# Kernel optimization log

Hardware: AMD Instinct MI355X
Metric: run time of the kernel (lower is better)

## Reference

```python
import jax, jax.numpy as jnp
import numpy as np

B, T, D_MODEL, WINDOW = 2, 2048, 512, 32


def setup_inputs() -> dict:
    key = jax.random.key(0)
    ks = jax.random.split(key, 5)
    s = 1.0 / np.sqrt(D_MODEL)
    x = jax.random.normal(ks[0], (B, T, D_MODEL), jnp.float32)
    # torch.nn.Linear convention: weight [out_features, in_features], y = x @ W.T + b
    w_qkv = jax.random.uniform(ks[1], (3 * D_MODEL, D_MODEL), jnp.float32, -s, s)
    b_qkv = jax.random.uniform(ks[2], (3 * D_MODEL,), jnp.float32, -s, s)
    w_proj = jax.random.uniform(ks[3], (D_MODEL, D_MODEL), jnp.float32, -s, s)
    b_proj = jax.random.uniform(ks[4], (D_MODEL,), jnp.float32, -s, s)
    return {"x": x, "w_qkv": w_qkv, "b_qkv": b_qkv, "w_proj": w_proj, "b_proj": b_proj}


def reference(x, w_qkv, b_qkv, w_proj, b_proj):
    Bb, Tt, C = x.shape
    qkv = x @ w_qkv.T + b_qkv                      # [B,T,3C]
    q, k, v = jnp.split(qkv, 3, axis=-1)           # each [B,T,C]
    W = 2 * WINDOW - 1                             # non-causal window span [t-w+1, t+w-1]
    offs = jnp.arange(W) - (WINDOW - 1)            # [W]
    idx = jnp.arange(Tt)[:, None] + offs[None, :]  # [T,W] absolute key positions
    valid = (idx >= 0) & (idx < Tt)                # mask out-of-range window slots
    idx_c = jnp.clip(idx, 0, Tt - 1)
    k_win = k[:, idx_c]                            # [B,T,W,C]
    v_win = v[:, idx_c]                            # [B,T,W,C]
    scale = jnp.asarray(C, x.dtype) ** 0.5
    scores = jnp.einsum('btc,btwc->btw', q, k_win) / scale
    scores = jnp.where(valid[None], scores, -jnp.inf)
    p = jax.nn.softmax(scores, axis=-1)            # [B,T,W]
    out = jnp.einsum('btw,btwc->btc', p, v_win)    # [B,T,C]
    return out @ w_proj.T + b_proj
```

## Files before the change

### kernel.cpp

```cpp
#include <hip/hip_runtime.h>
#include <math.h>

#define BB 2
#define TT 2048
#define CC 512
#define WIN 32
#define WSZ 63
#define MM (BB * TT)

typedef __attribute__((ext_vector_type(8))) short short8;
typedef __attribute__((ext_vector_type(4))) float floatx4;

__device__ inline unsigned short bf16_rn(float f) {
  unsigned u = __builtin_bit_cast(unsigned, f);
  u += 0x7fff + ((u >> 16) & 1);
  return (unsigned short)(u >> 16);
}
__device__ inline unsigned pack_bf16x2(float lo, float hi) {
  return (unsigned)bf16_rn(lo) | ((unsigned)bf16_rn(hi) << 16);
}

__device__ inline void gll16(const void* g, void* l) {
  __builtin_amdgcn_global_load_lds(
      (const __attribute__((address_space(1))) void*)g,
      (__attribute__((address_space(3))) void*)l, 16, 0, 0);
}

#define NX  (MM * CC)
#define NWQ (3 * CC * CC)
#define NWP (CC * CC)

__global__ __launch_bounds__(256) void convert_bf16(
    const float* __restrict__ x, const float* __restrict__ wq,
    const float* __restrict__ wp, ushort* __restrict__ xb,
    ushort* __restrict__ wqb, ushort* __restrict__ wpb) {
  const size_t e = ((size_t)blockIdx.x * 256 + threadIdx.x) * 8;
  const float* src;
  ushort* dst;
  size_t off;
  if (e < NX) { src = x; dst = xb; off = e; }
  else if (e < NX + NWQ) { src = wq; dst = wqb; off = e - NX; }
  else { src = wp; dst = wpb; off = e - NX - NWQ; }
  float4 v0 = ((const float4*)(src + off))[0];
  float4 v1 = ((const float4*)(src + off))[1];
  uint4 o;
  o.x = pack_bf16x2(v0.x, v0.y);
  o.y = pack_bf16x2(v0.z, v0.w);
  o.z = pack_bf16x2(v1.x, v1.y);
  o.w = pack_bf16x2(v1.z, v1.w);
  *(uint4*)(dst + off) = o;
}

#define GBK 32
#define VTBASE 1024

template <int BN, typename OT>
__global__ __launch_bounds__(256) void gemm_nt_mfma(
    const ushort* __restrict__ A, const ushort* __restrict__ B,
    const float* __restrict__ bias, OT* __restrict__ C,
    ushort* __restrict__ VT, int M, int N, int K) {
  constexpr int NI = 4;
  constexpr int MIW = (BN == 128) ? 4 : 2;
  __shared__ __align__(16) ushort As[128 * GBK];
  __shared__ __align__(16) ushort Bs[BN * GBK];

  const int tid = threadIdx.x;
  const int lane = tid & 63;
  const int wave = tid >> 6;
  const int wm = (BN == 128) ? (wave >> 1) * 64 : wave * 32;
  const int wn = (BN == 128) ? (wave & 1) * 64 : 0;
  const int m0 = blockIdx.y * 128;
  const int n0 = blockIdx.x * BN;
  const int mlane = lane & 15, quad = lane >> 4;
  const int lrow = lane >> 2, lcol = (lane & 3) * 8;

  floatx4 acc[MIW][NI];
#pragma unroll
  for (int i = 0; i < MIW; ++i)
#pragma unroll
    for (int j = 0; j < NI; ++j) acc[i][j] = (floatx4){0.f, 0.f, 0.f, 0.f};

  for (int k0 = 0; k0 < K; k0 += GBK) {
    __syncthreads();
#pragma unroll
    for (int q = 0; q < 2; ++q) {
      const int r0 = (q * 4 + wave) * 16;
      gll16(A + (size_t)(m0 + r0 + lrow) * K + k0 + lcol, As + r0 * GBK);
    }
#pragma unroll
    for (int q = 0; q < BN / 64; ++q) {
      const int r0 = (q * 4 + wave) * 16;
      gll16(B + (size_t)(n0 + r0 + lrow) * K + k0 + lcol, Bs + r0 * GBK);
    }
    __syncthreads();

    short8 af[MIW], bfr[NI];
#pragma unroll
    for (int mi = 0; mi < MIW; ++mi)
      af[mi] = *(const short8*)(&As[(wm + mi * 16 + mlane) * GBK + quad * 8]);
#pragma unroll
    for (int ni = 0; ni < NI; ++ni)
      bfr[ni] = *(const short8*)(&Bs[(wn + ni * 16 + mlane) * GBK + quad * 8]);
#pragma unroll
    for (int mi = 0; mi < MIW; ++mi)
#pragma unroll
      for (int ni = 0; ni < NI; ++ni)
        acc[mi][ni] = __builtin_amdgcn_mfma_f32_16x16x32_bf16(af[mi], bfr[ni], acc[mi][ni], 0, 0, 0);
  }

  const bool vpath = (VT != nullptr) && (n0 >= VTBASE);
#pragma unroll
  for (int ni = 0; ni < NI; ++ni) {
    const int n = n0 + wn + ni * 16 + mlane;
    const float bn = bias[n];
#pragma unroll
    for (int mi = 0; mi < MIW; ++mi) {
      const int mbase = m0 + wm + mi * 16 + quad * 4;
      if (vpath) {
        ushort4 pk;
        pk.x = bf16_rn(acc[mi][ni][0] + bn);
        pk.y = bf16_rn(acc[mi][ni][1] + bn);
        pk.z = bf16_rn(acc[mi][ni][2] + bn);
        pk.w = bf16_rn(acc[mi][ni][3] + bn);
        *(ushort4*)(VT + (size_t)(n - VTBASE) * M + mbase) = pk;
      } else {
#pragma unroll
        for (int r = 0; r < 4; ++r) {
          float val = acc[mi][ni][r] + bn;
          if constexpr (sizeof(OT) == 2)
            ((ushort*)C)[(size_t)(mbase + r) * N + n] = bf16_rn(val);
          else
            ((float*)C)[(size_t)(mbase + r) * N + n] = val;
        }
      }
    }
  }
}

#define ATILE 8
#define SLD 84
#define PLD 104

__global__ __launch_bounds__(256) void attn_mfma(
    const ushort* __restrict__ qkv, const ushort* __restrict__ vT,
    ushort* __restrict__ out) {
  __shared__ __align__(16) float s_s[16 * SLD];
  __shared__ __align__(16) ushort p_s[16 * PLD];

  const int tid = threadIdx.x;
  const int wave = tid >> 6, lane = tid & 63;
  const int mlane = lane & 15, quad = lane >> 4;
  const int bt0 = blockIdx.x * ATILE;
  const int b = bt0 / TT, t0 = bt0 % TT;
  const ushort* qbase = qkv + (size_t)b * TT * (3 * CC);

  const ushort* qrow  = qbase + (ptrdiff_t)(t0 + mlane) * (3 * CC);
  const ushort* krow0 = qbase + (ptrdiff_t)(t0 - 32 + wave * 16 + mlane) * (3 * CC) + CC;
  const ushort* krow1 = qbase + (ptrdiff_t)(t0 - 32 + 64 + mlane) * (3 * CC) + CC;
  floatx4 sacc0 = (floatx4){0.f, 0.f, 0.f, 0.f};
  floatx4 sacc1 = (floatx4){0.f, 0.f, 0.f, 0.f};
#pragma unroll
  for (int ks = 0; ks < 16; ++ks) {
    short8 a  = *(const short8*)(qrow + ks * 32 + quad * 8);
    short8 b0 = *(const short8*)(krow0 + ks * 32 + quad * 8);
    sacc0 = __builtin_amdgcn_mfma_f32_16x16x32_bf16(a, b0, sacc0, 0, 0, 0);
    if (wave == 0) {
      short8 b1 = *(const short8*)(krow1 + ks * 32 + quad * 8);
      sacc1 = __builtin_amdgcn_mfma_f32_16x16x32_bf16(a, b1, sacc1, 0, 0, 0);
    }
  }

#pragma unroll
  for (int r = 0; r < 4; ++r)
    s_s[(quad * 4 + r) * SLD + wave * 16 + mlane] = sacc0[r];
  if (wave == 0) {
#pragma unroll
    for (int r = 0; r < 4; ++r)
      s_s[(quad * 4 + r) * SLD + 64 + mlane] = sacc1[r];
  }
  __syncthreads();

  {
    const int row = tid >> 4, li = tid & 15;
    const float inv_scale = 0.044194173824159216f;
    float e[5];
    float mx = -INFINITY;
#pragma unroll
    for (int i = 0; i < 5; ++i) {
      const int r = li + 16 * i;
      const int j = r - 1 - row;
      const int src = t0 - 32 + r;
      const bool valid = (j >= 0) && (j < WSZ) && (src >= 0) && (src < TT);
      e[i] = valid ? s_s[row * SLD + r] * inv_scale : -INFINITY;
      mx = fmaxf(mx, e[i]);
    }
    mx = fmaxf(mx, __shfl_xor(mx, 1)); mx = fmaxf(mx, __shfl_xor(mx, 2));
    mx = fmaxf(mx, __shfl_xor(mx, 4)); mx = fmaxf(mx, __shfl_xor(mx, 8));
    float sum = 0.f;
#pragma unroll
    for (int i = 0; i < 5; ++i) {
      e[i] = (e[i] == -INFINITY) ? 0.f : __expf(e[i] - mx);
      sum += e[i];
    }
    sum += __shfl_xor(sum, 1); sum += __shfl_xor(sum, 2);
    sum += __shfl_xor(sum, 4); sum += __shfl_xor(sum, 8);
    const float rs = 1.f / sum;
#pragma unroll
    for (int i = 0; i < 5; ++i)
      p_s[row * PLD + li + 16 * i] = bf16_rn(e[i] * rs);
    if (li < 8) {
      p_s[row * PLD + 80 + li] = 0;
      p_s[row * PLD + 88 + li] = 0;
      p_s[row * PLD + 96 + li] = 0;
    }
  }
  __syncthreads();

  const ptrdiff_t mcol0 = (ptrdiff_t)b * TT + t0 - 32;
#pragma unroll 2
  for (int nt8 = 0; nt8 < 8; ++nt8) {
    const int nt = wave * 8 + nt8;
    const ushort* vrow = vT + (ptrdiff_t)(nt * 16 + mlane) * MM + mcol0;
    floatx4 o = (floatx4){0.f, 0.f, 0.f, 0.f};
#pragma unroll
    for (int ks = 0; ks < 3; ++ks) {
      short8 a  = *(const short8*)(&p_s[mlane * PLD + ks * 32 + quad * 8]);
      short8 bv = *(const short8*)(vrow + ks * 32 + quad * 8);
      o = __builtin_amdgcn_mfma_f32_16x16x32_bf16(a, bv, o, 0, 0, 0);
    }
    if (quad < 2) {
#pragma unroll
      for (int r = 0; r < 4; ++r)
        out[(size_t)(bt0 + quad * 4 + r) * CC + nt * 16 + mlane] = bf16_rn(o[r]);
    }
  }
}

extern "C" void kernel_launch(void* const* d_in, const int* in_sizes, int n_in,
                              void* d_out, int out_size, void* d_ws, size_t ws_size,
                              hipStream_t stream) {
  const float* x      = (const float*)d_in[0];
  const float* w_qkv  = (const float*)d_in[1];
  const float* b_qkv  = (const float*)d_in[2];
  const float* w_proj = (const float*)d_in[3];
  const float* b_proj = (const float*)d_in[4];
  float* outp = (float*)d_out;

  ushort* base  = (ushort*)d_ws;
  ushort* qkv   = base + 131072;
  ushort* attn  = qkv + (size_t)MM * 3 * CC;
  ushort* xb    = attn + (size_t)MM * CC;
  ushort* wqb   = xb + (size_t)NX;
  ushort* wpb   = wqb + (size_t)NWQ;
  ushort* vTg   = wpb + (size_t)NWP;
  ushort* vT    = vTg + 64;

  convert_bf16<<<(NX + NWQ + NWP) / (256 * 8), 256, 0, stream>>>(x, w_qkv, w_proj, xb, wqb, wpb);
  {
    dim3 grid((3 * CC) / 128, MM / 128);
    gemm_nt_mfma<128, ushort><<<grid, 256, 0, stream>>>(xb, wqb, b_qkv, qkv, vT, MM, 3 * CC, CC);
  }
  attn_mfma<<<MM / ATILE, 256, 0, stream>>>(qkv, vT, attn);
  {
    dim3 grid(CC / 64, MM / 128);
    gemm_nt_mfma<64, float><<<grid, 256, 0, stream>>>(attn, wpb, b_proj, outp, nullptr, MM, CC, CC);
  }
}
```

Before: 120.5 us.

## Replace GEMM with B-panel-in-LDS kernel reading A directly from global

Rewrites both GEMMs so each block stages a 64-row weight panel (half of K at a time) in padded LDS and streams A fragments straight from global memory into MFMA operands. This removes the per-K-step double barrier and small global-to-LDS loads. Tile shapes change to 128x64 for the QKV GEMM and 64x64 for the projection, which doubles the block count. The V-transpose epilogue now goes through LDS so VT gets coalesced 16-byte stores. The cost is uncached global reads of A with a 64-byte stride per lane, and lower arithmetic intensity per block.

```diff
diff --git a/kernel.cpp b/kernel.cpp
--- a/kernel.cpp
+++ b/kernel.cpp
@@ -18,12 +18,6 @@
 }
 __device__ inline unsigned pack_bf16x2(float lo, float hi) {
   return (unsigned)bf16_rn(lo) | ((unsigned)bf16_rn(hi) << 16);
-}
-
-__device__ inline void gll16(const void* g, void* l) {
-  __builtin_amdgcn_global_load_lds(
-      (const __attribute__((address_space(1))) void*)g,
-      (__attribute__((address_space(3))) void*)l, 16, 0, 0);
 }
 
 #define NX  (MM * CC)
@@ -51,79 +45,67 @@
   *(uint4*)(dst + off) = o;
 }
 
-#define GBK 32
-#define VTBASE 1024
-
-template <int BN, typename OT>
-__global__ __launch_bounds__(256) void gemm_nt_mfma(
+#define PSTR 264
+#define VSTR 136
+
+template <int BM, typename OT>
+__global__ __launch_bounds__(256) void gemm_panel(
     const ushort* __restrict__ A, const ushort* __restrict__ B,
     const float* __restrict__ bias, OT* __restrict__ C,
-    ushort* __restrict__ VT, int M, int N, int K) {
-  constexpr int NI = 4;
-  constexpr int MIW = (BN == 128) ? 4 : 2;
-  __shared__ __align__(16) ushort As[128 * GBK];
-  __shared__ __align__(16) ushort Bs[BN * GBK];
+    ushort* __restrict__ VT, int M, int N) {
+  constexpr int MIW = BM / 64;
+  __shared__ __align__(16) ushort Bs[64 * PSTR];
 
   const int tid = threadIdx.x;
   const int lane = tid & 63;
   const int wave = tid >> 6;
-  const int wm = (BN == 128) ? (wave >> 1) * 64 : wave * 32;
-  const int wn = (BN == 128) ? (wave & 1) * 64 : 0;
-  const int m0 = blockIdx.y * 128;
-  const int n0 = blockIdx.x * BN;
+  const int m0 = blockIdx.y * BM;
+  const int n0 = blockIdx.x * 64;
+  const int wm = wave * (BM / 4);
   const int mlane = lane & 15, quad = lane >> 4;
-  const int lrow = lane >> 2, lcol = (lane & 3) * 8;
-
-  floatx4 acc[MIW][NI];
+
+  floatx4 acc[MIW][4];
 #pragma unroll
   for (int i = 0; i < MIW; ++i)
 #pragma unroll
-    for (int j = 0; j < NI; ++j) acc[i][j] = (floatx4){0.f, 0.f, 0.f, 0.f};
-
-  for (int k0 = 0; k0 < K; k0 += GBK) {
+    for (int j = 0; j < 4; ++j) acc[i][j] = (floatx4){0.f, 0.f, 0.f, 0.f};
+
+  for (int h = 0; h < 2; ++h) {
+    if (h) __syncthreads();
+#pragma unroll
+    for (int i = 0; i < 8; ++i) {
+      const int idx = tid + 256 * i;
+      const int r = idx >> 5, kc = (idx & 31) * 8;
+      *(uint4*)(&Bs[r * PSTR + kc]) =
+          *(const uint4*)(B + (size_t)(n0 + r) * CC + h * 256 + kc);
+    }
     __syncthreads();
 #pragma unroll
-    for (int q = 0; q < 2; ++q) {
-      const int r0 = (q * 4 + wave) * 16;
-      gll16(A + (size_t)(m0 + r0 + lrow) * K + k0 + lcol, As + r0 * GBK);
-    }
-#pragma unroll
-    for (int q = 0; q < BN / 64; ++q) {
-      const int r0 = (q * 4 + wave) * 16;
-      gll16(B + (size_t)(n0 + r0 + lrow) * K + k0 + lcol, Bs + r0 * GBK);
-    }
-    __syncthreads();
-
-    short8 af[MIW], bfr[NI];
-#pragma unroll
-    for (int mi = 0; mi < MIW; ++mi)
-      af[mi] = *(const short8*)(&As[(wm + mi * 16 + mlane) * GBK + quad * 8]);
-#pragma unroll
-    for (int ni = 0; ni < NI; ++ni)
-      bfr[ni] = *(const short8*)(&Bs[(wn + ni * 16 + mlane) * GBK + quad * 8]);
-#pragma unroll
-    for (int mi = 0; mi < MIW; ++mi)
-#pragma unroll
-      for (int ni = 0; ni < NI; ++ni)
-        acc[mi][ni] = __builtin_amdgcn_mfma_f32_16x16x32_bf16(af[mi], bfr[ni], acc[mi][ni], 0, 0, 0);
-  }
-
-  const bool vpath = (VT != nullptr) && (n0 >= VTBASE);
-#pragma unroll
-  for (int ni = 0; ni < NI; ++ni) {
-    const int n = n0 + wn + ni * 16 + mlane;
-    const float bn = bias[n];
-#pragma unroll
-    for (int mi = 0; mi < MIW; ++mi) {
-      const int mbase = m0 + wm + mi * 16 + quad * 4;
-      if (vpath) {
-        ushort4 pk;
-        pk.x = bf16_rn(acc[mi][ni][0] + bn);
-        pk.y = bf16_rn(acc[mi][ni][1] + bn);
-        pk.z = bf16_rn(acc[mi][ni][2] + bn);
-        pk.w = bf16_rn(acc[mi][ni][3] + bn);
-        *(ushort4*)(VT + (size_t)(n - VTBASE) * M + mbase) = pk;
-      } else {
+    for (int ks = 0; ks < 8; ++ks) {
+      short8 bfr[4];
+#pragma unroll
+      for (int ni = 0; ni < 4; ++ni)
+        bfr[ni] = *(const short8*)(&Bs[(ni * 16 + mlane) * PSTR + ks * 32 + quad * 8]);
+#pragma unroll
+      for (int mi = 0; mi < MIW; ++mi) {
+        short8 af = *(const short8*)(
+            A + (size_t)(m0 + wm + mi * 16 + mlane) * CC + h * 256 + ks * 32 + quad * 8);
+#pragma unroll
+        for (int ni = 0; ni < 4; ++ni)
+          acc[mi][ni] = __builtin_amdgcn_mfma_f32_16x16x32_bf16(af, bfr[ni], acc[mi][ni], 0, 0, 0);
+      }
+    }
+  }
+
+  const bool vpath = (VT != nullptr) && (n0 >= 1024);
+  if (!vpath) {
+#pragma unroll
+    for (int ni = 0; ni < 4; ++ni) {
+      const int n = n0 + ni * 16 + mlane;
+      const float bn = bias[n];
+#pragma unroll
+      for (int mi = 0; mi < MIW; ++mi) {
+        const int mbase = m0 + wm + mi * 16 + quad * 4;
 #pragma unroll
         for (int r = 0; r < 4; ++r) {
           float val = acc[mi][ni][r] + bn;
@@ -133,6 +115,32 @@
             ((float*)C)[(size_t)(mbase + r) * N + n] = val;
         }
       }
+    }
+  } else if constexpr (BM == 128) {
+    ushort* Vt = Bs;
+    __syncthreads();
+#pragma unroll
+    for (int ni = 0; ni < 4; ++ni) {
+      const int n_l = ni * 16 + mlane;
+      const float bn = bias[n0 + n_l];
+#pragma unroll
+      for (int mi = 0; mi < MIW; ++mi) {
+        const int m_l = wm + mi * 16 + quad * 4;
+        ushort4 pk;
+        pk.x = bf16_rn(acc[mi][ni][0] + bn);
+        pk.y = bf16_rn(acc[mi][ni][1] + bn);
+        pk.z = bf16_rn(acc[mi][ni][2] + bn);
+        pk.w = bf16_rn(acc[mi][ni][3] + bn);
+        *(ushort4*)(&Vt[n_l * VSTR + m_l]) = pk;
+      }
+    }
+    __syncthreads();
+#pragma unroll
+    for (int i = 0; i < 4; ++i) {
+      const int idx = tid + 256 * i;
+      const int n_l = idx >> 4, mo = (idx & 15) * 8;
+      *(uint4*)(VT + (size_t)(n0 - 1024 + n_l) * M + m0 + mo) =
+          *(const uint4*)(&Vt[n_l * VSTR + mo]);
     }
   }
 }
@@ -257,12 +265,12 @@
 
   convert_bf16<<<(NX + NWQ + NWP) / (256 * 8), 256, 0, stream>>>(x, w_qkv, w_proj, xb, wqb, wpb);
   {
-    dim3 grid((3 * CC) / 128, MM / 128);
-    gemm_nt_mfma<128, ushort><<<grid, 256, 0, stream>>>(xb, wqb, b_qkv, qkv, vT, MM, 3 * CC, CC);
+    dim3 grid((3 * CC) / 64, MM / 128);
+    gemm_panel<128, ushort><<<grid, 256, 0, stream>>>(xb, wqb, b_qkv, qkv, vT, MM, 3 * CC);
   }
   attn_mfma<<<MM / ATILE, 256, 0, stream>>>(qkv, vT, attn);
   {
-    dim3 grid(CC / 64, MM / 128);
-    gemm_nt_mfma<64, float><<<grid, 256, 0, stream>>>(attn, wpb, b_proj, outp, nullptr, MM, CC, CC);
-  }
-}
+    dim3 grid(CC / 64, MM / 64);
+    gemm_panel<64, float><<<grid, 256, 0, stream>>>(attn, wpb, b_proj, outp, nullptr, MM, CC);
+  }
+}
```

After: 114.9 us. 4.7% less time.
